# Kernel tuning notes

Hardware: AMD Instinct MI355X
Metric: run time of the kernel (lower is better)

The kernel has to match this reference:

```python
import jax, jax.numpy as jnp
import numpy as np

N = 512
B = 128
T = 1000
INP = 6
OUT = 1
DT, TAU = 1.0, 10.0
ALPHA = DT / TAU
SIGMA_REC, SIGMA_INP = 0.05, 0.01
SPECTRAL_RAD = 1.2


def setup_inputs() -> dict:
    key = jax.random.key(0)
    k_u, k_rn, k_in, k_wr, k_wi, k_wo = jax.random.split(key, 6)
    u = jax.random.normal(k_u, (B, T, INP), dtype=jnp.float32)
    # noise pre-scaled as in the torch module: sqrt(2/alpha * sigma^2) * randn
    rec_noise = jnp.sqrt(2.0 / ALPHA * SIGMA_REC ** 2) * jax.random.normal(k_rn, (B, T, N), dtype=jnp.float32)
    inp_noise = jnp.sqrt(2.0 / ALPHA * SIGMA_INP ** 2) * jax.random.normal(k_in, (B, T, INP), dtype=jnp.float32)
    # scaled init connectivity (stand-in for get_connectivity): spectral radius ~ SPECTRAL_RAD
    W_rec = (SPECTRAL_RAD / np.sqrt(N)) * jax.random.normal(k_wr, (N, N), dtype=jnp.float32)
    W_inp = (1.0 / np.sqrt(INP)) * jax.random.normal(k_wi, (N, INP), dtype=jnp.float32)
    W_out = (1.0 / np.sqrt(N)) * jax.random.normal(k_wo, (OUT, N), dtype=jnp.float32)
    y_init = jnp.zeros((N,), dtype=jnp.float32)
    return {"u": u, "rec_noise": rec_noise, "inp_noise": inp_noise,
            "W_rec": W_rec, "W_inp": W_inp, "W_out": W_out, "y_init": y_init}


def _run_dynamics(u, rec_noise, inp_noise, W_rec, W_inp, W_out, y_init):
    alpha = jnp.float32(ALPHA)
    s0 = jnp.broadcast_to(y_init, (u.shape[0], N))  # (B, N)

    def step(s, xs):
        u_t, in_t, rn_t = xs  # (B,INP),(B,INP),(B,N)
        pre = s @ W_rec.T + (u_t + in_t) @ W_inp.T
        s_new = (1.0 - alpha) * s + alpha * (jax.nn.relu(pre) + rn_t)
        return s_new, s_new

    # torch loop runs for i in range(T-1); step i uses inputs/noise at time i
    xs = (jnp.swapaxes(u[:, :-1], 0, 1),
          jnp.swapaxes(inp_noise[:, :-1], 0, 1),
          jnp.swapaxes(rec_noise[:, :-1], 0, 1))
    _, states_tail = jax.lax.scan(step, s0, xs)  # (T-1, B, N)
    states = jnp.concatenate([s0[:, None, :], jnp.swapaxes(states_tail, 0, 1)], axis=1)  # (B, T, N)
    outputs = states @ W_out.T  # (B, T, OUT)
    return states, outputs


def reference(u, rec_noise, inp_noise, W_rec, W_inp, W_out, y_init):
    return _run_dynamics(u, rec_noise, inp_noise, W_rec, W_inp, W_out, y_init)
```

## Files before the change

### kernel.cpp

```cpp
#include <hip/hip_runtime.h>


#define NN 512
#define BB 128
#define TT 1000
#define NIN 6
#define PP 4
#define GG 4
#define NGRP (BB / GG)
#define NWG (PP * NGRP)
#define SLICE (NN / PP)
#define XWORDS (2 * NGRP * GG * NN)
#define WS_NEED (XWORDS * sizeof(unsigned long long))

typedef unsigned long long u64;

__global__ void init_xbuf(u64* xbuf) {
  const int i = blockIdx.x * 256 + threadIdx.x;
  if (i < XWORDS / 2) {
    reinterpret_cast<u64*>(xbuf)[i] = 0xFFFFFFFF00000000ULL;
    reinterpret_cast<u64*>(xbuf)[i + XWORDS / 2] = 0xFFFFFFFF00000000ULL;
  }
}

__device__ __forceinline__ float wave_sum(float v) {
  #pragma unroll
  for (int off = 32; off > 0; off >>= 1) v += __shfl_xor(v, off, 64);
  return v;
}

__device__ __forceinline__ void pin4(float4& a, float4& b, float4& c, float4& d) {
  asm volatile("" : "+v"(a.x), "+v"(a.y), "+v"(a.z), "+v"(a.w),
                    "+v"(b.x), "+v"(b.y), "+v"(b.z), "+v"(b.w),
                    "+v"(c.x), "+v"(c.y), "+v"(c.z), "+v"(c.w),
                    "+v"(d.x), "+v"(d.y), "+v"(d.z), "+v"(d.w));
}

__device__ __forceinline__ u64 xld(const u64* p) {
  return __hip_atomic_load(p, __ATOMIC_RELAXED, __HIP_MEMORY_SCOPE_SYSTEM);
}
__device__ __forceinline__ void xst(u64* p, u64 v) {
  __hip_atomic_store(p, v, __ATOMIC_RELAXED, __HIP_MEMORY_SCOPE_SYSTEM);
}

__global__ __launch_bounds__(512, 1)
void rnn_tagx(const float* __restrict__ u, const float* __restrict__ rnz,
              const float* __restrict__ inz, const float* __restrict__ Wrec,
              const float* __restrict__ Winp, const float* __restrict__ yinit,
              float* __restrict__ states, u64* __restrict__ xbuf) {
  const int tid = threadIdx.x;
  const int xcd = blockIdx.x & 7;
  const int rest = blockIdx.x >> 3;
  const int p = rest & 3;
  const int g = (rest >> 2) * 8 + xcd;

  const int nq = tid & 31;
  const int n0 = nq << 2;
  const int ks = tid >> 5;
  const int k0 = ks << 5;
  const int ub = tid >> 7;
  const int un = tid & 127;
  const int ung = p * SLICE + un;

  __shared__ __align__(16) float pred[16][GG][SLICE];
  __shared__ __align__(16) float s_all[GG][NN];
  __shared__ float winp_s[SLICE][NIN];
  __shared__ float ubuf[2][GG][NIN];

  float4 w[4][8];
  #pragma unroll
  for (int i = 0; i < 4; ++i) {
    const float* wr = Wrec + (size_t)(p * SLICE + n0 + i) * NN + k0;
    #pragma unroll
    for (int q = 0; q < 8; ++q)
      w[i][q] = *reinterpret_cast<const float4*>(wr + 4 * q);
  }
  for (int i = tid; i < SLICE * NIN; i += 512) {
    const int r = i / NIN, j = i - r * NIN;
    winp_s[r][j] = Winp[(p * SLICE + r) * NIN + j];
  }
  for (int i = tid; i < GG * NN; i += 512)
    s_all[i >> 9][i & 511] = yinit[i & 511];
  float scur = yinit[ung];
  states[(size_t)(g * GG + ub) * TT * NN + ung] = scur;
  __syncthreads();

  for (int t = 0; t < TT - 1; ++t) {
    const int par = t & 1;

    #pragma unroll
    for (int i = 0; i < 4; ++i) {
      pin4(w[i][0], w[i][1], w[i][2], w[i][3]);
      pin4(w[i][4], w[i][5], w[i][6], w[i][7]);
    }

    const float rnv = rnz[((size_t)(g * GG + ub) * TT + t) * NN + ung];
    if (tid < GG * NIN) {
      const int b = tid / NIN, j = tid - b * NIN;
      const size_t idx = ((size_t)(g * GG + b) * TT + t) * NIN + j;
      ubuf[par][b][j] = u[idx] + inz[idx];
    }

    if (t > 0) {
      const u64* xb = xbuf + (((size_t)par * NGRP + g) * GG + ub) * NN;
      const int q0 = (p + 1) & 3, q1 = (p + 2) & 3, q2 = (p + 3) & 3;
      const u64* p0 = xb + q0 * SLICE + un;
      const u64* p1 = xb + q1 * SLICE + un;
      const u64* p2 = xb + q2 * SLICE + un;
      u64 v0 = xld(p0), v1 = xld(p1), v2 = xld(p2);
      while ((int)(v0 >> 32) < t) { __builtin_amdgcn_s_sleep(1); v0 = xld(p0); }
      while ((int)(v1 >> 32) < t) { __builtin_amdgcn_s_sleep(1); v1 = xld(p1); }
      while ((int)(v2 >> 32) < t) { __builtin_amdgcn_s_sleep(1); v2 = xld(p2); }
      s_all[ub][q0 * SLICE + un] = __uint_as_float((unsigned)v0);
      s_all[ub][q1 * SLICE + un] = __uint_as_float((unsigned)v1);
      s_all[ub][q2 * SLICE + un] = __uint_as_float((unsigned)v2);
    }
    __syncthreads();

    float a0[GG], a1[GG], a2[GG], a3[GG];
    #pragma unroll
    for (int b = 0; b < GG; ++b) { a0[b] = 0.f; a1[b] = 0.f; a2[b] = 0.f; a3[b] = 0.f; }
    #pragma unroll
    for (int b = 0; b < GG; ++b) {
      #pragma unroll
      for (int q = 0; q < 8; ++q) {
        const float4 sv = *reinterpret_cast<const float4*>(&s_all[b][k0 + 4 * q]);
        a0[b] = fmaf(w[0][q].x, sv.x, a0[b]); a0[b] = fmaf(w[0][q].y, sv.y, a0[b]);
        a0[b] = fmaf(w[0][q].z, sv.z, a0[b]); a0[b] = fmaf(w[0][q].w, sv.w, a0[b]);
        a1[b] = fmaf(w[1][q].x, sv.x, a1[b]); a1[b] = fmaf(w[1][q].y, sv.y, a1[b]);
        a1[b] = fmaf(w[1][q].z, sv.z, a1[b]); a1[b] = fmaf(w[1][q].w, sv.w, a1[b]);
        a2[b] = fmaf(w[2][q].x, sv.x, a2[b]); a2[b] = fmaf(w[2][q].y, sv.y, a2[b]);
        a2[b] = fmaf(w[2][q].z, sv.z, a2[b]); a2[b] = fmaf(w[2][q].w, sv.w, a2[b]);
        a3[b] = fmaf(w[3][q].x, sv.x, a3[b]); a3[b] = fmaf(w[3][q].y, sv.y, a3[b]);
        a3[b] = fmaf(w[3][q].z, sv.z, a3[b]); a3[b] = fmaf(w[3][q].w, sv.w, a3[b]);
      }
    }
    #pragma unroll
    for (int b = 0; b < GG; ++b)
      *reinterpret_cast<float4*>(&pred[ks][b][n0]) =
          make_float4(a0[b], a1[b], a2[b], a3[b]);
    __syncthreads();

    {
      float pre = 0.f;
      #pragma unroll
      for (int q = 0; q < 16; ++q) pre += pred[q][ub][un];
      #pragma unroll
      for (int j = 0; j < NIN; ++j)
        pre = fmaf(ubuf[par][ub][j], winp_s[un][j], pre);
      const float sn = 0.9f * scur + 0.1f * (fmaxf(pre, 0.f) + rnv);
      states[((size_t)(g * GG + ub) * TT + t + 1) * NN + ung] = sn;
      const u64 pw = ((u64)(unsigned)(t + 1) << 32) | __float_as_uint(sn);
      xst(&xbuf[(((size_t)((t + 1) & 1) * NGRP + g) * GG + ub) * NN + ung], pw);
      asm volatile("" ::: "memory");
      s_all[ub][ung] = sn;
      scur = sn;
    }
  }
}

__global__ __launch_bounds__(256)
void out_proj(const float* __restrict__ states, const float* __restrict__ Wout,
              float* __restrict__ outputs) {
  const int lane = threadIdx.x & 63;
  const size_t row = (size_t)blockIdx.x * 4 + (threadIdx.x >> 6);
  if (row >= (size_t)BB * TT) return;
  const float* sr = states + row * NN;
  float acc = 0.f;
  #pragma unroll
  for (int h = 0; h < 2; ++h) {
    const float4 sv = *reinterpret_cast<const float4*>(sr + h * 256 + lane * 4);
    const float4 wv = *reinterpret_cast<const float4*>(Wout + h * 256 + lane * 4);
    acc = fmaf(sv.x, wv.x, acc);
    acc = fmaf(sv.y, wv.y, acc);
    acc = fmaf(sv.z, wv.z, acc);
    acc = fmaf(sv.w, wv.w, acc);
  }
  acc = wave_sum(acc);
  if (lane == 0) outputs[row] = acc;
}

__global__ __launch_bounds__(512)
void rnn_fused(const float* __restrict__ u, const float* __restrict__ rnz,
               const float* __restrict__ inz, const float* __restrict__ Wsrc,
               const float* __restrict__ Winp, const float* __restrict__ Wout,
               const float* __restrict__ yinit,
               float* __restrict__ states, float* __restrict__ outputs) {
  const int tid = threadIdx.x;
  const int n4 = tid & 127;
  const int kc = tid >> 7;
  const int b0 = blockIdx.x * 2;
  const int b1 = b0 + 1;

  __shared__ __align__(16) float s[2][NN];
  __shared__ __align__(16) float red[2][128][20];
  __shared__ float ubf[2 * NIN];
  __shared__ float outred[2][8];

  float wi[NIN];
  #pragma unroll
  for (int j = 0; j < NIN; ++j) wi[j] = Winp[tid * NIN + j];
  const float wo = Wout[tid];
  const float yv = yinit[tid];

  s[0][tid] = yv;
  s[1][tid] = yv;
  states[(size_t)(b0 * TT) * NN + tid] = yv;
  states[(size_t)(b1 * TT) * NN + tid] = yv;
  {
    float pzz = wave_sum(yv * wo);
    if ((tid & 63) == 0) outred[0][tid >> 6] = pzz;
  }
  __syncthreads();
  if (tid < 2) {
    float a = 0.f;
    #pragma unroll
    for (int wq = 0; wq < 8; ++wq) a += outred[0][wq];
    outputs[(tid ? b1 : b0) * TT] = a;
  }
  __syncthreads();

  for (int t = 0; t < TT - 1; ++t) {
    const float rn0 = rnz[(size_t)(b0 * TT + t) * NN + tid];
    const float rn1 = rnz[(size_t)(b1 * TT + t) * NN + tid];
    float uv = 0.f;
    if (tid < 2 * NIN) {
      const int b = (tid < NIN) ? b0 : b1;
      const int j = (tid < NIN) ? tid : tid - NIN;
      const int idx = (b * TT + t) * NIN + j;
      uv = u[idx] + inz[idx];
    }
    float a0[4] = {0.f, 0.f, 0.f, 0.f};
    float a1[4] = {0.f, 0.f, 0.f, 0.f};
    const int kbase0 = kc * 128;
    #pragma unroll 4
    for (int j4 = 0; j4 < 32; ++j4) {
      const int kb = kbase0 + j4 * 4;
      const float4 s0v = *reinterpret_cast<const float4*>(&s[0][kb]);
      const float4 s1v = *reinterpret_cast<const float4*>(&s[1][kb]);
      const float s0a[4] = {s0v.x, s0v.y, s0v.z, s0v.w};
      const float s1a[4] = {s1v.x, s1v.y, s1v.z, s1v.w};
      #pragma unroll
      for (int jj = 0; jj < 4; ++jj) {
        const int k = kb + jj;
        const float* pw = Wsrc + (size_t)(n4 << 2) * NN + k;
        float4 wv;
        wv.x = pw[0]; wv.y = pw[NN]; wv.z = pw[2 * NN]; wv.w = pw[3 * NN];
        a0[0] = fmaf(wv.x, s0a[jj], a0[0]);
        a0[1] = fmaf(wv.y, s0a[jj], a0[1]);
        a0[2] = fmaf(wv.z, s0a[jj], a0[2]);
        a0[3] = fmaf(wv.w, s0a[jj], a0[3]);
        a1[0] = fmaf(wv.x, s1a[jj], a1[0]);
        a1[1] = fmaf(wv.y, s1a[jj], a1[1]);
        a1[2] = fmaf(wv.z, s1a[jj], a1[2]);
        a1[3] = fmaf(wv.w, s1a[jj], a1[3]);
      }
    }
    if (tid < 2 * NIN) ubf[tid] = uv;
    *reinterpret_cast<float4*>(&red[0][n4][kc << 2]) =
        make_float4(a0[0], a0[1], a0[2], a0[3]);
    *reinterpret_cast<float4*>(&red[1][n4][kc << 2]) =
        make_float4(a1[0], a1[1], a1[2], a1[3]);
    __syncthreads();
    const int n = tid;
    const int r = n >> 2, c = n & 3;
    float pre0 = (red[0][r][c] + red[0][r][4 + c]) +
                 (red[0][r][8 + c] + red[0][r][12 + c]);
    float pre1 = (red[1][r][c] + red[1][r][4 + c]) +
                 (red[1][r][8 + c] + red[1][r][12 + c]);
    #pragma unroll
    for (int j = 0; j < NIN; ++j) {
      pre0 = fmaf(ubf[j], wi[j], pre0);
      pre1 = fmaf(ubf[NIN + j], wi[j], pre1);
    }
    const float sn0 = 0.9f * s[0][n] + 0.1f * (fmaxf(pre0, 0.f) + rn0);
    const float sn1 = 0.9f * s[1][n] + 0.1f * (fmaxf(pre1, 0.f) + rn1);
    states[(size_t)(b0 * TT + t + 1) * NN + n] = sn0;
    states[(size_t)(b1 * TT + t + 1) * NN + n] = sn1;
    s[0][n] = sn0;
    s[1][n] = sn1;
    float p0 = wave_sum(sn0 * wo);
    float p1 = wave_sum(sn1 * wo);
    if ((tid & 63) == 0) {
      outred[0][tid >> 6] = p0;
      outred[1][tid >> 6] = p1;
    }
    __syncthreads();
    if (tid < 2) {
      float a = 0.f;
      #pragma unroll
      for (int wq = 0; wq < 8; ++wq) a += outred[tid][wq];
      outputs[(tid ? b1 : b0) * TT + t + 1] = a;
    }
  }
}

extern "C" void kernel_launch(void* const* d_in, const int* in_sizes, int n_in,
                              void* d_out, int out_size, void* d_ws, size_t ws_size,
                              hipStream_t stream) {
  const float* u    = (const float*)d_in[0];
  const float* rnz  = (const float*)d_in[1];
  const float* inz  = (const float*)d_in[2];
  const float* Wrec = (const float*)d_in[3];
  const float* Winp = (const float*)d_in[4];
  const float* Wout = (const float*)d_in[5];
  const float* yin  = (const float*)d_in[6];
  float* states  = (float*)d_out;
  float* outputs = states + (size_t)BB * TT * NN;

  if (ws_size >= WS_NEED) {
    u64* xbuf = (u64*)d_ws;
    init_xbuf<<<(XWORDS / 2 + 255) / 256, 256, 0, stream>>>(xbuf);
    rnn_tagx<<<NWG, 512, 0, stream>>>(u, rnz, inz, Wrec, Winp, yin,
                                      states, xbuf);
    out_proj<<<(BB * TT + 3) / 4, 256, 0, stream>>>(states, Wout, outputs);
  } else {
    rnn_fused<<<BB / 2, 512, 0, stream>>>(u, rnz, inz, Wrec, Winp, Wout,
                                          yin, states, outputs);
  }
}
```

Before: 2.988 ms.

## Split each batch group into two skewed halves to overlap exchange with compute

Each workgroup's four batch rows are split into two halves processed in alternating phases. While one half's matvec runs, the cross-workgroup state exchange for the other half is in flight, so polling latency can overlap with compute. This also prefetches the tagged xbuf values before spinning. The cost is twice the barriers per timestep and half-width matvec phases, which may lower ALU utilisation and add more synchronisation overhead.

After: 3.414 ms. 14.2% more time.

```diff
diff --git a/kernel.cpp b/kernel.cpp
--- a/kernel.cpp
+++ b/kernel.cpp
@@ -18,8 +18,8 @@
 __global__ void init_xbuf(u64* xbuf) {
   const int i = blockIdx.x * 256 + threadIdx.x;
   if (i < XWORDS / 2) {
-    reinterpret_cast<u64*>(xbuf)[i] = 0xFFFFFFFF00000000ULL;
-    reinterpret_cast<u64*>(xbuf)[i + XWORDS / 2] = 0xFFFFFFFF00000000ULL;
+    xbuf[i] = 0xFFFFFFFF00000000ULL;
+    xbuf[i + XWORDS / 2] = 0xFFFFFFFF00000000ULL;
   }
 }
 
@@ -44,7 +44,7 @@
 }
 
 __global__ __launch_bounds__(512, 1)
-void rnn_tagx(const float* __restrict__ u, const float* __restrict__ rnz,
+void rnn_skew(const float* __restrict__ u, const float* __restrict__ rnz,
               const float* __restrict__ inz, const float* __restrict__ Wrec,
               const float* __restrict__ Winp, const float* __restrict__ yinit,
               float* __restrict__ states, u64* __restrict__ xbuf) {
@@ -58,14 +58,20 @@
   const int n0 = nq << 2;
   const int ks = tid >> 5;
   const int k0 = ks << 5;
-  const int ub = tid >> 7;
+  const int ubh = (tid >> 7) & 1;
   const int un = tid & 127;
   const int ung = p * SLICE + un;
-
-  __shared__ __align__(16) float pred[16][GG][SLICE];
+  const int q1 = (p + 1 + (tid >> 8)) & 3;
+  const int fb1 = (tid & 255) >> 7;
+  const int fun1 = tid & 127;
+  const int q2 = (p + 3) & 3;
+  const int fb2 = (tid >> 7) & 1;
+  const int fun2 = tid & 127;
+
+  __shared__ __align__(16) float pred[16][2][SLICE];
   __shared__ __align__(16) float s_all[GG][NN];
   __shared__ float winp_s[SLICE][NIN];
-  __shared__ float ubuf[2][GG][NIN];
+  __shared__ float ubuf[GG][NIN];
 
   float4 w[4][8];
   #pragma unroll
@@ -81,12 +87,20 @@
   }
   for (int i = tid; i < GG * NN; i += 512)
     s_all[i >> 9][i & 511] = yinit[i & 511];
-  float scur = yinit[ung];
-  states[(size_t)(g * GG + ub) * TT * NN + ung] = scur;
+  {
+    const int b = tid >> 7;
+    states[(size_t)(g * GG + b) * TT * NN + ung] = yinit[ung];
+  }
+  float scurA = yinit[ung];
+  float scurB = scurA;
   __syncthreads();
+
+  u64 pfA = 0, pfB = 0;
 
   for (int t = 0; t < TT - 1; ++t) {
     const int par = t & 1;
+    const u64* xbr = xbuf + ((size_t)par * NGRP + g) * GG * NN;
+    u64* xbw = xbuf + ((size_t)((t + 1) & 1) * NGRP + g) * GG * NN;
 
     #pragma unroll
     for (int i = 0; i < 4; ++i) {
@@ -94,67 +108,131 @@
       pin4(w[i][4], w[i][5], w[i][6], w[i][7]);
     }
 
-    const float rnv = rnz[((size_t)(g * GG + ub) * TT + t) * NN + ung];
+    float rnzA = 0.f, rnzB = 0.f;
+    if (tid < 256) {
+      rnzA = rnz[((size_t)(g * GG + ubh) * TT + t) * NN + ung];
+      rnzB = rnz[((size_t)(g * GG + 2 + ubh) * TT + t) * NN + ung];
+    }
     if (tid < GG * NIN) {
       const int b = tid / NIN, j = tid - b * NIN;
       const size_t idx = ((size_t)(g * GG + b) * TT + t) * NIN + j;
-      ubuf[par][b][j] = u[idx] + inz[idx];
+      ubuf[b][j] = u[idx] + inz[idx];
     }
 
     if (t > 0) {
-      const u64* xb = xbuf + (((size_t)par * NGRP + g) * GG + ub) * NN;
-      const int q0 = (p + 1) & 3, q1 = (p + 2) & 3, q2 = (p + 3) & 3;
-      const u64* p0 = xb + q0 * SLICE + un;
-      const u64* p1 = xb + q1 * SLICE + un;
-      const u64* p2 = xb + q2 * SLICE + un;
-      u64 v0 = xld(p0), v1 = xld(p1), v2 = xld(p2);
-      while ((int)(v0 >> 32) < t) { __builtin_amdgcn_s_sleep(1); v0 = xld(p0); }
-      while ((int)(v1 >> 32) < t) { __builtin_amdgcn_s_sleep(1); v1 = xld(p1); }
-      while ((int)(v2 >> 32) < t) { __builtin_amdgcn_s_sleep(1); v2 = xld(p2); }
-      s_all[ub][q0 * SLICE + un] = __uint_as_float((unsigned)v0);
-      s_all[ub][q1 * SLICE + un] = __uint_as_float((unsigned)v1);
-      s_all[ub][q2 * SLICE + un] = __uint_as_float((unsigned)v2);
-    }
-    __syncthreads();
-
-    float a0[GG], a1[GG], a2[GG], a3[GG];
-    #pragma unroll
-    for (int b = 0; b < GG; ++b) { a0[b] = 0.f; a1[b] = 0.f; a2[b] = 0.f; a3[b] = 0.f; }
-    #pragma unroll
-    for (int b = 0; b < GG; ++b) {
-      #pragma unroll
-      for (int q = 0; q < 8; ++q) {
-        const float4 sv = *reinterpret_cast<const float4*>(&s_all[b][k0 + 4 * q]);
-        a0[b] = fmaf(w[0][q].x, sv.x, a0[b]); a0[b] = fmaf(w[0][q].y, sv.y, a0[b]);
-        a0[b] = fmaf(w[0][q].z, sv.z, a0[b]); a0[b] = fmaf(w[0][q].w, sv.w, a0[b]);
-        a1[b] = fmaf(w[1][q].x, sv.x, a1[b]); a1[b] = fmaf(w[1][q].y, sv.y, a1[b]);
-        a1[b] = fmaf(w[1][q].z, sv.z, a1[b]); a1[b] = fmaf(w[1][q].w, sv.w, a1[b]);
-        a2[b] = fmaf(w[2][q].x, sv.x, a2[b]); a2[b] = fmaf(w[2][q].y, sv.y, a2[b]);
-        a2[b] = fmaf(w[2][q].z, sv.z, a2[b]); a2[b] = fmaf(w[2][q].w, sv.w, a2[b]);
-        a3[b] = fmaf(w[3][q].x, sv.x, a3[b]); a3[b] = fmaf(w[3][q].y, sv.y, a3[b]);
-        a3[b] = fmaf(w[3][q].z, sv.z, a3[b]); a3[b] = fmaf(w[3][q].w, sv.w, a3[b]);
-      }
-    }
-    #pragma unroll
-    for (int b = 0; b < GG; ++b)
-      *reinterpret_cast<float4*>(&pred[ks][b][n0]) =
-          make_float4(a0[b], a1[b], a2[b], a3[b]);
-    __syncthreads();
+      const u64* a1p = xbr + fb1 * NN + q1 * SLICE + fun1;
+      int tg = (int)(pfA >> 32);
+      while (tg < t) { __builtin_amdgcn_s_sleep(1); pfA = xld(a1p); tg = (int)(pfA >> 32); }
+      s_all[fb1][q1 * SLICE + fun1] = __uint_as_float((unsigned)pfA);
+      if (tid < 256) {
+        const u64* a2p = xbr + fb2 * NN + q2 * SLICE + fun2;
+        tg = (int)(pfB >> 32);
+        while (tg < t) { __builtin_amdgcn_s_sleep(1); pfB = xld(a2p); tg = (int)(pfB >> 32); }
+        s_all[fb2][q2 * SLICE + fun2] = __uint_as_float((unsigned)pfB);
+      }
+    }
+    __syncthreads();
+
+    if (t > 0) {
+      pfA = xld(xbr + (2 + fb1) * NN + q1 * SLICE + fun1);
+      if (tid < 256) pfB = xld(xbr + (2 + fb2) * NN + q2 * SLICE + fun2);
+      asm volatile("" ::: "memory");
+    }
 
     {
+      float a0[2], a1[2], a2[2], a3[2];
+      #pragma unroll
+      for (int bh = 0; bh < 2; ++bh) { a0[bh] = 0.f; a1[bh] = 0.f; a2[bh] = 0.f; a3[bh] = 0.f; }
+      #pragma unroll
+      for (int bh = 0; bh < 2; ++bh) {
+        #pragma unroll
+        for (int q = 0; q < 8; ++q) {
+          const float4 sv = *reinterpret_cast<const float4*>(&s_all[bh][k0 + 4 * q]);
+          a0[bh] = fmaf(w[0][q].x, sv.x, a0[bh]); a0[bh] = fmaf(w[0][q].y, sv.y, a0[bh]);
+          a0[bh] = fmaf(w[0][q].z, sv.z, a0[bh]); a0[bh] = fmaf(w[0][q].w, sv.w, a0[bh]);
+          a1[bh] = fmaf(w[1][q].x, sv.x, a1[bh]); a1[bh] = fmaf(w[1][q].y, sv.y, a1[bh]);
+          a1[bh] = fmaf(w[1][q].z, sv.z, a1[bh]); a1[bh] = fmaf(w[1][q].w, sv.w, a1[bh]);
+          a2[bh] = fmaf(w[2][q].x, sv.x, a2[bh]); a2[bh] = fmaf(w[2][q].y, sv.y, a2[bh]);
+          a2[bh] = fmaf(w[2][q].z, sv.z, a2[bh]); a2[bh] = fmaf(w[2][q].w, sv.w, a2[bh]);
+          a3[bh] = fmaf(w[3][q].x, sv.x, a3[bh]); a3[bh] = fmaf(w[3][q].y, sv.y, a3[bh]);
+          a3[bh] = fmaf(w[3][q].z, sv.z, a3[bh]); a3[bh] = fmaf(w[3][q].w, sv.w, a3[bh]);
+        }
+        *reinterpret_cast<float4*>(&pred[ks][bh][n0]) =
+            make_float4(a0[bh], a1[bh], a2[bh], a3[bh]);
+      }
+    }
+    __syncthreads();
+
+    if (tid < 256) {
       float pre = 0.f;
       #pragma unroll
-      for (int q = 0; q < 16; ++q) pre += pred[q][ub][un];
-      #pragma unroll
-      for (int j = 0; j < NIN; ++j)
-        pre = fmaf(ubuf[par][ub][j], winp_s[un][j], pre);
-      const float sn = 0.9f * scur + 0.1f * (fmaxf(pre, 0.f) + rnv);
-      states[((size_t)(g * GG + ub) * TT + t + 1) * NN + ung] = sn;
-      const u64 pw = ((u64)(unsigned)(t + 1) << 32) | __float_as_uint(sn);
-      xst(&xbuf[(((size_t)((t + 1) & 1) * NGRP + g) * GG + ub) * NN + ung], pw);
+      for (int q = 0; q < 16; ++q) pre += pred[q][ubh][un];
+      #pragma unroll
+      for (int j = 0; j < NIN; ++j) pre = fmaf(ubuf[ubh][j], winp_s[un][j], pre);
+      const float sn = 0.9f * scurA + 0.1f * (fmaxf(pre, 0.f) + rnzA);
+      states[((size_t)(g * GG + ubh) * TT + t + 1) * NN + ung] = sn;
+      xst(xbw + ubh * NN + ung,
+          ((u64)(unsigned)(t + 1) << 32) | __float_as_uint(sn));
+      s_all[ubh][ung] = sn;
+      scurA = sn;
+    }
+
+    if (t > 0) {
+      const u64* a1p = xbr + (2 + fb1) * NN + q1 * SLICE + fun1;
+      int tg = (int)(pfA >> 32);
+      while (tg < t) { __builtin_amdgcn_s_sleep(1); pfA = xld(a1p); tg = (int)(pfA >> 32); }
+      s_all[2 + fb1][q1 * SLICE + fun1] = __uint_as_float((unsigned)pfA);
+      if (tid < 256) {
+        const u64* a2p = xbr + (2 + fb2) * NN + q2 * SLICE + fun2;
+        tg = (int)(pfB >> 32);
+        while (tg < t) { __builtin_amdgcn_s_sleep(1); pfB = xld(a2p); tg = (int)(pfB >> 32); }
+        s_all[2 + fb2][q2 * SLICE + fun2] = __uint_as_float((unsigned)pfB);
+      }
+    }
+    __syncthreads();
+
+    {
+      pfA = xld((const u64*)xbw + fb1 * NN + q1 * SLICE + fun1);
+      if (tid < 256) pfB = xld((const u64*)xbw + fb2 * NN + q2 * SLICE + fun2);
       asm volatile("" ::: "memory");
-      s_all[ub][ung] = sn;
-      scur = sn;
+    }
+
+    {
+      float a0[2], a1[2], a2[2], a3[2];
+      #pragma unroll
+      for (int bh = 0; bh < 2; ++bh) { a0[bh] = 0.f; a1[bh] = 0.f; a2[bh] = 0.f; a3[bh] = 0.f; }
+      #pragma unroll
+      for (int bh = 0; bh < 2; ++bh) {
+        #pragma unroll
+        for (int q = 0; q < 8; ++q) {
+          const float4 sv = *reinterpret_cast<const float4*>(&s_all[2 + bh][k0 + 4 * q]);
+          a0[bh] = fmaf(w[0][q].x, sv.x, a0[bh]); a0[bh] = fmaf(w[0][q].y, sv.y, a0[bh]);
+          a0[bh] = fmaf(w[0][q].z, sv.z, a0[bh]); a0[bh] = fmaf(w[0][q].w, sv.w, a0[bh]);
+          a1[bh] = fmaf(w[1][q].x, sv.x, a1[bh]); a1[bh] = fmaf(w[1][q].y, sv.y, a1[bh]);
+          a1[bh] = fmaf(w[1][q].z, sv.z, a1[bh]); a1[bh] = fmaf(w[1][q].w, sv.w, a1[bh]);
+          a2[bh] = fmaf(w[2][q].x, sv.x, a2[bh]); a2[bh] = fmaf(w[2][q].y, sv.y, a2[bh]);
+          a2[bh] = fmaf(w[2][q].z, sv.z, a2[bh]); a2[bh] = fmaf(w[2][q].w, sv.w, a2[bh]);
+          a3[bh] = fmaf(w[3][q].x, sv.x, a3[bh]); a3[bh] = fmaf(w[3][q].y, sv.y, a3[bh]);
+          a3[bh] = fmaf(w[3][q].z, sv.z, a3[bh]); a3[bh] = fmaf(w[3][q].w, sv.w, a3[bh]);
+        }
+        *reinterpret_cast<float4*>(&pred[ks][bh][n0]) =
+            make_float4(a0[bh], a1[bh], a2[bh], a3[bh]);
+      }
+    }
+    __syncthreads();
+
+    if (tid < 256) {
+      float pre = 0.f;
+      #pragma unroll
+      for (int q = 0; q < 16; ++q) pre += pred[q][ubh][un];
+      #pragma unroll
+      for (int j = 0; j < NIN; ++j) pre = fmaf(ubuf[2 + ubh][j], winp_s[un][j], pre);
+      const float sn = 0.9f * scurB + 0.1f * (fmaxf(pre, 0.f) + rnzB);
+      states[((size_t)(g * GG + 2 + ubh) * TT + t + 1) * NN + ung] = sn;
+      xst(xbw + (2 + ubh) * NN + ung,
+          ((u64)(unsigned)(t + 1) << 32) | __float_as_uint(sn));
+      s_all[2 + ubh][ung] = sn;
+      scurB = sn;
     }
   }
 }
@@ -311,7 +389,7 @@
   if (ws_size >= WS_NEED) {
     u64* xbuf = (u64*)d_ws;
     init_xbuf<<<(XWORDS / 2 + 255) / 256, 256, 0, stream>>>(xbuf);
-    rnn_tagx<<<NWG, 512, 0, stream>>>(u, rnz, inz, Wrec, Winp, yin,
+    rnn_skew<<<NWG, 512, 0, stream>>>(u, rnz, inz, Wrec, Winp, yin,
                                       states, xbuf);
     out_proj<<<(BB * TT + 3) / 4, 256, 0, stream>>>(states, Wout, outputs);
   } else {
```

## Halve batch group per workgroup to double workgroup count in persistent RNN

Applied to the files above, without the earlier changes.

Reduces the number of batch rows handled by each workgroup from 4 to 2, so the grid grows from 128 to 256 persistent workgroups and per-step work per workgroup shrinks. The cross-workgroup state exchange, finalize stage and initial state writes are remapped so only half the threads produce outputs while all threads help poll the exchange buffer. Each workgroup still loads the same weight slice, and twice as many spinning workgroups add flag-polling traffic while the finalize stage leaves half the threads idle.

Measured after the change: 2.862 ms. 4.2% less time.

```diff
diff --git a/kernel.cpp b/kernel.cpp
--- a/kernel.cpp
+++ b/kernel.cpp
@@ -6,7 +6,7 @@
 #define TT 1000
 #define NIN 6
 #define PP 4
-#define GG 4
+#define GG 2
 #define NGRP (BB / GG)
 #define NWG (PP * NGRP)
 #define SLICE (NN / PP)
@@ -18,8 +18,8 @@
 __global__ void init_xbuf(u64* xbuf) {
   const int i = blockIdx.x * 256 + threadIdx.x;
   if (i < XWORDS / 2) {
-    reinterpret_cast<u64*>(xbuf)[i] = 0xFFFFFFFF00000000ULL;
-    reinterpret_cast<u64*>(xbuf)[i + XWORDS / 2] = 0xFFFFFFFF00000000ULL;
+    xbuf[i] = 0xFFFFFFFF00000000ULL;
+    xbuf[i + XWORDS / 2] = 0xFFFFFFFF00000000ULL;
   }
 }
 
@@ -44,10 +44,10 @@
 }
 
 __global__ __launch_bounds__(512, 1)
-void rnn_tagx(const float* __restrict__ u, const float* __restrict__ rnz,
-              const float* __restrict__ inz, const float* __restrict__ Wrec,
-              const float* __restrict__ Winp, const float* __restrict__ yinit,
-              float* __restrict__ states, u64* __restrict__ xbuf) {
+void rnn_tagx2(const float* __restrict__ u, const float* __restrict__ rnz,
+               const float* __restrict__ inz, const float* __restrict__ Wrec,
+               const float* __restrict__ Winp, const float* __restrict__ yinit,
+               float* __restrict__ states, u64* __restrict__ xbuf) {
   const int tid = threadIdx.x;
   const int xcd = blockIdx.x & 7;
   const int rest = blockIdx.x >> 3;
@@ -58,9 +58,13 @@
   const int n0 = nq << 2;
   const int ks = tid >> 5;
   const int k0 = ks << 5;
-  const int ub = tid >> 7;
+  const int ub = (tid >> 7) & 1;
   const int un = tid & 127;
   const int ung = p * SLICE + un;
+  const int f1r = tid >> 8, f1b = (tid >> 7) & 1, f1n = tid & 127;
+  const int f1q = (p + 1 + f1r) & 3;
+  const int f2b = (tid >> 7) & 1, f2n = tid & 127;
+  const int f2q = (p + 3) & 3;
 
   __shared__ __align__(16) float pred[16][GG][SLICE];
   __shared__ __align__(16) float s_all[GG][NN];
@@ -81,8 +85,9 @@
   }
   for (int i = tid; i < GG * NN; i += 512)
     s_all[i >> 9][i & 511] = yinit[i & 511];
-  float scur = yinit[ung];
-  states[(size_t)(g * GG + ub) * TT * NN + ung] = scur;
+  for (int i = tid; i < GG * NN; i += 512)
+    states[(size_t)(g * GG + (i >> 9)) * TT * NN + (i & 511)] = yinit[i & 511];
+  float scur = (tid < 256) ? yinit[ung] : 0.f;
   __syncthreads();
 
   for (int t = 0; t < TT - 1; ++t) {
@@ -94,7 +99,9 @@
       pin4(w[i][4], w[i][5], w[i][6], w[i][7]);
     }
 
-    const float rnv = rnz[((size_t)(g * GG + ub) * TT + t) * NN + ung];
+    float rnv = 0.f;
+    if (tid < 256)
+      rnv = rnz[((size_t)(g * GG + ub) * TT + t) * NN + ung];
     if (tid < GG * NIN) {
       const int b = tid / NIN, j = tid - b * NIN;
       const size_t idx = ((size_t)(g * GG + b) * TT + t) * NIN + j;
@@ -102,18 +109,18 @@
     }
 
     if (t > 0) {
-      const u64* xb = xbuf + (((size_t)par * NGRP + g) * GG + ub) * NN;
-      const int q0 = (p + 1) & 3, q1 = (p + 2) & 3, q2 = (p + 3) & 3;
-      const u64* p0 = xb + q0 * SLICE + un;
-      const u64* p1 = xb + q1 * SLICE + un;
-      const u64* p2 = xb + q2 * SLICE + un;
-      u64 v0 = xld(p0), v1 = xld(p1), v2 = xld(p2);
-      while ((int)(v0 >> 32) < t) { __builtin_amdgcn_s_sleep(1); v0 = xld(p0); }
+      const u64* xb = xbuf + ((size_t)par * NGRP + g) * GG * NN;
+      const u64* p1 = xb + (size_t)f1b * NN + f1q * SLICE + f1n;
+      u64 v1 = xld(p1);
+      u64 v2 = 0;
+      const u64* p2 = xb + (size_t)f2b * NN + f2q * SLICE + f2n;
+      if (tid < 256) v2 = xld(p2);
       while ((int)(v1 >> 32) < t) { __builtin_amdgcn_s_sleep(1); v1 = xld(p1); }
-      while ((int)(v2 >> 32) < t) { __builtin_amdgcn_s_sleep(1); v2 = xld(p2); }
-      s_all[ub][q0 * SLICE + un] = __uint_as_float((unsigned)v0);
-      s_all[ub][q1 * SLICE + un] = __uint_as_float((unsigned)v1);
-      s_all[ub][q2 * SLICE + un] = __uint_as_float((unsigned)v2);
+      s_all[f1b][f1q * SLICE + f1n] = __uint_as_float((unsigned)v1);
+      if (tid < 256) {
+        while ((int)(v2 >> 32) < t) { __builtin_amdgcn_s_sleep(1); v2 = xld(p2); }
+        s_all[f2b][f2q * SLICE + f2n] = __uint_as_float((unsigned)v2);
+      }
     }
     __syncthreads();
 
@@ -141,7 +148,7 @@
           make_float4(a0[b], a1[b], a2[b], a3[b]);
     __syncthreads();
 
-    {
+    if (tid < 256) {
       float pre = 0.f;
       #pragma unroll
       for (int q = 0; q < 16; ++q) pre += pred[q][ub][un];
@@ -311,8 +318,8 @@
   if (ws_size >= WS_NEED) {
     u64* xbuf = (u64*)d_ws;
     init_xbuf<<<(XWORDS / 2 + 255) / 256, 256, 0, stream>>>(xbuf);
-    rnn_tagx<<<NWG, 512, 0, stream>>>(u, rnz, inz, Wrec, Winp, yin,
-                                      states, xbuf);
+    rnn_tagx2<<<NWG, 512, 0, stream>>>(u, rnz, inz, Wrec, Winp, yin,
+                                       states, xbuf);
     out_proj<<<(BB * TT + 3) / 4, 256, 0, stream>>>(states, Wout, outputs);
   } else {
     rnn_fused<<<BB / 2, 512, 0, stream>>>(u, rnz, inz, Wrec, Winp, Wout,
```
